# Optimization experiments

Measured on AMD Instinct MI355X. Metric: run time of the kernel, lower is better.

Reference implementation:

```python
import jax, jax.numpy as jnp
import numpy as np

D = 4096       # embed_dim
H = 16         # num_heads
HD = D // H    # head_dim = 256
MLP_H = int(D * 2.0)  # 8192
L_V = 2048
L_T = 1024
GAMMA = 0.6
NOISE_STD = 0.07
TEMP = 0.05
LN_EPS = 1e-5


def setup_inputs() -> dict:
    key = jax.random.key(0)
    ks = jax.random.split(key, 16)
    s = 0.02
    return {
        "vision_feature": jax.random.normal(ks[0], (L_V, D), jnp.float32),
        "text_embed": jax.random.normal(ks[1], (L_T, D), jnp.float32),
        "attention_mask": jnp.zeros((L_T,), jnp.float32),  # additive mask, 0 = attend
        "noise": jax.random.normal(ks[2], (L_V,), jnp.float32),
        "Wq": jax.random.normal(ks[3], (D, D), jnp.float32) * s,
        "bq": jnp.zeros((D,), jnp.float32),
        "Wk": jax.random.normal(ks[4], (D, D), jnp.float32) * s,
        "bk": jnp.zeros((D,), jnp.float32),
        "Wv": jax.random.normal(ks[5], (D, D), jnp.float32) * s,
        "bv": jnp.zeros((D,), jnp.float32),
        "Wo": jax.random.normal(ks[6], (D, D), jnp.float32) * s,
        "bo": jnp.zeros((D,), jnp.float32),
        "ln_w": jnp.ones((D,), jnp.float32),
        "ln_b": jnp.zeros((D,), jnp.float32),
        "W1": jax.random.normal(ks[7], (MLP_H, D), jnp.float32) * s,
        "b1": jnp.zeros((MLP_H,), jnp.float32),
        "W2": jax.random.normal(ks[8], (1, MLP_H), jnp.float32) * s,
        "b2": jnp.zeros((1,), jnp.float32),
    }


def reference(vision_feature, text_embed, attention_mask, noise,
              Wq, bq, Wk, bk, Wv, bv, Wo, bo, ln_w, ln_b, W1, b1, W2, b2):
    # --- cross attention (vision queries over text keys/values) ---
    q = (vision_feature @ Wq.T + bq).reshape(L_V, H, HD)
    k = (text_embed @ Wk.T + bk).reshape(L_T, H, HD)
    v = (text_embed @ Wv.T + bv).reshape(L_T, H, HD)
    logits = jnp.einsum('qhd,khd->hqk', q, k) / np.float32(np.sqrt(HD))
    logits = logits + attention_mask[None, None, :]  # additive attn_mask
    attn = jax.nn.softmax(logits, axis=-1)
    ctx = jnp.einsum('hqk,khd->qhd', attn, v).reshape(L_V, D)
    attn_out = ctx @ Wo.T + bo
    # --- residual + layernorm ---
    x = vision_feature + attn_out
    mu = jnp.mean(x, axis=-1, keepdims=True)
    var = jnp.mean(jnp.square(x - mu), axis=-1, keepdims=True)
    xn = (x - mu) / jnp.sqrt(var + LN_EPS) * ln_w + ln_b
    # --- tiny MLP scorer ---
    h = jax.nn.gelu(xn @ W1.T + b1, approximate=False)
    weight_scores = (h @ W2.T + b2)[:, 0] + noise * NOISE_STD
    # --- temperature softmax over all tokens, top-p (gamma) selection ---
    p = jax.nn.softmax(weight_scores / TEMP, axis=0)
    order = jnp.argsort(-p)           # descending sort indices
    cum = jnp.cumsum(p[order])
    keep = cum <= GAMMA               # threshold_index prefix mask
    gathered = vision_feature[order]  # [L_V, D]
    # fixed-shape stand-in for indices[:threshold_index] gather:
    # valid selected rows are the nonzero prefix
    return jnp.where(keep[:, None], gathered, jnp.zeros((), gathered.dtype))
```

## Files before the change

kernel.cpp:

```cpp
#include <hip/hip_runtime.h>
#include <math.h>


#define LV   2048
#define LT   1024
#define DIM  4096
#define NHD  16
#define HDD  256
#define MLPH 8192

typedef __attribute__((ext_vector_type(8))) short bfx8;
typedef __attribute__((ext_vector_type(4))) float fx4;
typedef unsigned short u16;

__device__ __forceinline__ float wave_sum(float v){
#pragma unroll
  for (int o = 32; o > 0; o >>= 1) v += __shfl_xor(v, o);
  return v;
}
__device__ __forceinline__ float wave_max(float v){
#pragma unroll
  for (int o = 32; o > 0; o >>= 1) v = fmaxf(v, __shfl_xor(v, o));
  return v;
}

__device__ __forceinline__ void splitpack(const float4 a, const float4 b,
                                          bfx8* hi, bfx8* lo){
  float f[8] = {a.x,a.y,a.z,a.w, b.x,b.y,b.z,b.w};
  union { bfx8 v; unsigned u[4]; } H, L;
#pragma unroll
  for (int p = 0; p < 4; ++p){
    unsigned u0 = __float_as_uint(f[2*p]);
    unsigned u1 = __float_as_uint(f[2*p+1]);
    H.u[p] = (u0 >> 16) | (u1 & 0xffff0000u);
    float h0 = __uint_as_float(u0 & 0xffff0000u);
    float h1 = __uint_as_float(u1 & 0xffff0000u);
    unsigned v0 = __float_as_uint(f[2*p]   - h0);
    unsigned v1 = __float_as_uint(f[2*p+1] - h1);
    L.u[p] = (v0 >> 16) | (v1 & 0xffff0000u);
  }
  *hi = H.v; *lo = L.v;
}

__device__ __forceinline__ void glds16(const void* g, void* l){
  __builtin_amdgcn_global_load_lds(
      (const __attribute__((address_space(1))) unsigned int*)g,
      (__attribute__((address_space(3))) unsigned int*)l, 16, 0, 0);
}

__global__ __launch_bounds__(256)
void repack_kernel(const float* __restrict__ src, u16* __restrict__ hi,
                   u16* __restrict__ lo, int Kc, int ktsh)
{
  const long long e = ((long long)blockIdx.x * 256 + threadIdx.x) * 8;
  const int T = (int)(e >> 9);
  const int L = (int)(e >> 3) & 63;
  const int rt = T >> ktsh, kt = T & ((1 << ktsh) - 1);
  const int r = (rt << 4) + (L & 15);
  const int k = (kt << 5) + ((L >> 4) << 3);
  const float* p = src + (long long)r * Kc + k;
  bfx8 h, l;
  splitpack(*(const float4*)p, *(const float4*)(p + 4), &h, &l);
  *(bfx8*)(hi + e) = h;
  *(bfx8*)(lo + e) = l;
}

template<int GELU, int TRANSC>
__global__ __launch_bounds__(256)
void mgemm(const u16* __restrict__ Ah, const u16* __restrict__ Al, int aKT, long long aZe,
           const u16* __restrict__ Bh, const u16* __restrict__ Bl, int bKT, long long bZe,
           float* __restrict__ C, int ldc, long long cZe,
           const float* __restrict__ bias,
           int nx, int KT, int kt0, int zkt, float alpha)
{
  __shared__ bfx8 lbuf[2][32][64];
  const int tid  = threadIdx.x;
  const int lane = tid & 63;
  const int wv   = tid >> 6;
  const int wr   = wv >> 1, wc = wv & 1;
  const int nwg  = gridDim.x;
  const int id   = blockIdx.x;
  int bm, bn;
  {
    const int my = nwg / nx;
    if (((nx & 3) == 0) && ((my & 1) == 0) && ((nwg & 7) == 0)){
      const int rm = my >> 1, rn = nx >> 2;
      const int x  = id & 7;
      const int j  = id >> 3;
      bm = ((x >> 2) * rm) + j / rn;
      bn = ((x & 3) * rn) + j % rn;
    } else if (((my & 7) == 0) && ((nwg & 7) == 0)){
      const int rm = my >> 3;
      const int x = id & 7, j = id >> 3;
      bm = x * rm + j / nx;
      bn = j % nx;
    } else { bm = id / nx; bn = id % nx; }
  }
  const int m0 = bm << 7;
  const int n0 = bn << 7;
  const int z    = blockIdx.z;
  const u16* Ahz = Ah + (long long)z * aZe;
  const u16* Alz = Al + (long long)z * aZe;
  const u16* Bhz = Bh + (long long)z * bZe;
  const u16* Blz = Bl + (long long)z * bZe;
  C += (long long)z * cZe;
  const int ktb  = kt0 + z * zkt;
  const int rtA0 = m0 >> 4, rtB0 = n0 >> 4;

  const fx4 zz = {0.f, 0.f, 0.f, 0.f};
  fx4 acc[4][4];
#pragma unroll
  for (int i = 0; i < 4; ++i)
#pragma unroll
    for (int j = 0; j < 4; ++j) acc[i][j] = zz;

  const u16* wbase = (wv == 0) ? Ahz : (wv == 1) ? Alz : (wv == 2) ? Bhz : Blz;
  const int  wrt0  = (wv < 2) ? rtA0 : rtB0;
  const int  wKT   = (wv < 2) ? aKT  : bKT;

#define STAGE(BUF, KTI)                                                        \
  {                                                                            \
    _Pragma("unroll")                                                          \
    for (int q = 0; q < 8; ++q){                                               \
      const u16* g = wbase + ((long long)(wrt0 + q) * wKT + (KTI)) * 512       \
                     + lane * 8;                                               \
      glds16((const void*)g, (void*)&lbuf[BUF][wv * 8 + q][0]);                \
    }                                                                          \
  }

  int cur = 0;
  STAGE(0, ktb);
  for (int t = 0; t < KT; ++t){
    __syncthreads();
    if (t + 1 < KT) STAGE(cur ^ 1, ktb + t + 1);
    bfx8 ah[4], al[4], bh[4], bl[4];
#pragma unroll
    for (int i = 0; i < 4; ++i){
      ah[i] = lbuf[cur][     wr*4 + i][lane];
      al[i] = lbuf[cur][ 8 + wr*4 + i][lane];
      bh[i] = lbuf[cur][16 + wc*4 + i][lane];
      bl[i] = lbuf[cur][24 + wc*4 + i][lane];
    }
#pragma unroll
    for (int i = 0; i < 4; ++i)
#pragma unroll
      for (int j = 0; j < 4; ++j){
        acc[i][j] = __builtin_amdgcn_mfma_f32_16x16x32_bf16(ah[i], bl[j], acc[i][j], 0, 0, 0);
        acc[i][j] = __builtin_amdgcn_mfma_f32_16x16x32_bf16(al[i], bh[j], acc[i][j], 0, 0, 0);
        acc[i][j] = __builtin_amdgcn_mfma_f32_16x16x32_bf16(ah[i], bh[j], acc[i][j], 0, 0, 0);
      }
    cur ^= 1;
  }
#undef STAGE

#pragma unroll
  for (int i = 0; i < 4; ++i){
    const int row0 = m0 + wr*64 + i*16 + ((lane >> 4) << 2);
#pragma unroll
    for (int j = 0; j < 4; ++j){
      const int col = n0 + wc*64 + j*16 + (lane & 15);
      const float bb = bias ? bias[col] : 0.0f;
      if (TRANSC){
        float4 o;
        o.x = alpha*acc[i][j][0] + bb;
        o.y = alpha*acc[i][j][1] + bb;
        o.z = alpha*acc[i][j][2] + bb;
        o.w = alpha*acc[i][j][3] + bb;
        *(float4*)(C + (size_t)col*ldc + row0) = o;
      } else {
#pragma unroll
        for (int r = 0; r < 4; ++r){
          float v = alpha*acc[i][j][r] + bb;
          if (GELU) v = 0.5f*v*(1.0f + erff(v*0.70710678f));
          C[(size_t)(row0 + r)*ldc + col] = v;
        }
      }
    }
  }
}

template<int GELU, int TRANSC>
__global__ __launch_bounds__(256)
void mgemm_fb(const float* __restrict__ A, long long aZ, int lda,
              const float* __restrict__ B, long long bZ, int ldb,
              float* __restrict__ C, long long cZ, int ldc,
              const float* __restrict__ bias, int Kd, float alpha)
{
  __shared__ bfx8 AhS[512], AlS[512], BhS[512], BlS[512];
  const int tid  = threadIdx.x;
  const int lane = tid & 63;
  const int wv   = tid >> 6;
  const int wr   = wv >> 1, wc = wv & 1;
  const int m0 = blockIdx.y * 128, n0 = blockIdx.x * 128;
  A += (long long)blockIdx.z * aZ;
  B += (long long)blockIdx.z * bZ;
  C += (long long)blockIdx.z * cZ;

  const fx4 zz = {0.f, 0.f, 0.f, 0.f};
  fx4 acc[4][4];
#pragma unroll
  for (int i = 0; i < 4; ++i)
#pragma unroll
    for (int j = 0; j < 4; ++j) acc[i][j] = zz;

  for (int k0 = 0; k0 < Kd; k0 += 32){
    __syncthreads();
#pragma unroll
    for (int pass = 0; pass < 2; ++pass){
      const int s = pass*256 + tid;
      const int m = ((s >> 6) << 4) + (s & 15);
      const int j = (s >> 4) & 3;
      const float* pA = A + (size_t)(m0 + m)*lda + k0 + j*8;
      splitpack(*(const float4*)pA, *(const float4*)(pA + 4), &AhS[s], &AlS[s]);
      const float* pB = B + (size_t)(n0 + m)*ldb + k0 + j*8;
      splitpack(*(const float4*)pB, *(const float4*)(pB + 4), &BhS[s], &BlS[s]);
    }
    __syncthreads();
    bfx8 ah[4], al[4], bh[4], bl[4];
#pragma unroll
    for (int i = 0; i < 4; ++i){
      ah[i] = AhS[(wr*4 + i)*64 + lane];
      al[i] = AlS[(wr*4 + i)*64 + lane];
      bh[i] = BhS[(wc*4 + i)*64 + lane];
      bl[i] = BlS[(wc*4 + i)*64 + lane];
    }
#pragma unroll
    for (int i = 0; i < 4; ++i)
#pragma unroll
      for (int j = 0; j < 4; ++j){
        acc[i][j] = __builtin_amdgcn_mfma_f32_16x16x32_bf16(ah[i], bl[j], acc[i][j], 0, 0, 0);
        acc[i][j] = __builtin_amdgcn_mfma_f32_16x16x32_bf16(al[i], bh[j], acc[i][j], 0, 0, 0);
        acc[i][j] = __builtin_amdgcn_mfma_f32_16x16x32_bf16(ah[i], bh[j], acc[i][j], 0, 0, 0);
      }
  }
#pragma unroll
  for (int i = 0; i < 4; ++i){
    const int row0 = m0 + wr*64 + i*16 + ((lane >> 4) << 2);
#pragma unroll
    for (int j = 0; j < 4; ++j){
      const int col = n0 + wc*64 + j*16 + (lane & 15);
      const float bb = bias ? bias[col] : 0.0f;
      if (TRANSC){
        float4 o;
        o.x = alpha*acc[i][j][0] + bb;
        o.y = alpha*acc[i][j][1] + bb;
        o.z = alpha*acc[i][j][2] + bb;
        o.w = alpha*acc[i][j][3] + bb;
        *(float4*)(C + (size_t)col*ldc + row0) = o;
      } else {
#pragma unroll
        for (int r = 0; r < 4; ++r){
          float v = alpha*acc[i][j][r] + bb;
          if (GELU) v = 0.5f*v*(1.0f + erff(v*0.70710678f));
          C[(size_t)(row0 + r)*ldc + col] = v;
        }
      }
    }
  }
}

__global__ __launch_bounds__(128)
void softmax_pack(const float* __restrict__ Lf, u16* __restrict__ ph,
                  u16* __restrict__ pl)
{
  __shared__ float rr[4];
  const int tid = threadIdx.x;
  const int h = blockIdx.x >> 11;
  const int m = blockIdx.x & 2047;
  const float* row = Lf + ((long long)h * 2048 + m) * 1024;
  const int k = tid * 8;
  float4 a = *(const float4*)(row + k);
  float4 b = *(const float4*)(row + k + 4);
  float v[8] = {a.x,a.y,a.z,a.w, b.x,b.y,b.z,b.w};
  float mx = v[0];
#pragma unroll
  for (int i = 1; i < 8; ++i) mx = fmaxf(mx, v[i]);
  mx = wave_max(mx);
  if ((tid & 63) == 0) rr[tid >> 6] = mx;
  __syncthreads();
  const float M = fmaxf(rr[0], rr[1]);
  float e[8], s = 0.0f;
#pragma unroll
  for (int i = 0; i < 8; ++i){ e[i] = expf(v[i] - M); s += e[i]; }
  s = wave_sum(s);
  if ((tid & 63) == 0) rr[2 + (tid >> 6)] = s;
  __syncthreads();
  const float S = rr[2] + rr[3];
  float4 p0 = make_float4(e[0]/S, e[1]/S, e[2]/S, e[3]/S);
  float4 p1 = make_float4(e[4]/S, e[5]/S, e[6]/S, e[7]/S);
  bfx8 hh, ll;
  splitpack(p0, p1, &hh, &ll);
  const int tile = (m >> 4) * 32 + (k >> 5);
  const int Lw = ((k >> 3) & 3) * 16 + (m & 15);
  const long long eoff = (long long)h * (2048ll*1024) + (long long)tile * 512 + Lw * 8;
  *(bfx8*)(ph + eoff) = hh;
  *(bfx8*)(pl + eoff) = ll;
}

__global__ __launch_bounds__(256)
void softmax_fb(float* __restrict__ X)
{
  __shared__ float r[8];
  const int tid = threadIdx.x;
  float* row = X + (size_t)blockIdx.x * 1024;
  float4 v = ((const float4*)row)[tid];
  float m = fmaxf(fmaxf(v.x,v.y), fmaxf(v.z,v.w));
  m = wave_max(m);
  if ((tid & 63) == 0) r[tid >> 6] = m;
  __syncthreads();
  m = fmaxf(fmaxf(r[0],r[1]), fmaxf(r[2],r[3]));
  float e0 = expf(v.x - m), e1 = expf(v.y - m), e2 = expf(v.z - m), e3 = expf(v.w - m);
  float s = (e0 + e1) + (e2 + e3);
  s = wave_sum(s);
  if ((tid & 63) == 0) r[4 + (tid >> 6)] = s;
  __syncthreads();
  s = (r[4] + r[5]) + (r[6] + r[7]);
  ((float4*)row)[tid] = make_float4(e0/s, e1/s, e2/s, e3/s);
}

template<int PACK>
__global__ __launch_bounds__(256)
void ln_kernel(const float* __restrict__ vis, const float* ao, float* xnf,
               u16* __restrict__ xh, u16* __restrict__ xl,
               const float* __restrict__ w, const float* __restrict__ b)
{
  __shared__ float r[8];
  __shared__ float stat[2];
  const int tid = threadIdx.x;
  const int m = blockIdx.x;
  const size_t base = (size_t)m * DIM + tid * 16;
  float x[16];
#pragma unroll
  for (int q = 0; q < 4; ++q){
    float4 a = *(const float4*)(vis + base + q*4);
    float4 c = *(const float4*)(ao  + base + q*4);
    x[q*4+0]=a.x+c.x; x[q*4+1]=a.y+c.y; x[q*4+2]=a.z+c.z; x[q*4+3]=a.w+c.w;
  }
  float s = 0.0f;
#pragma unroll
  for (int i = 0; i < 16; ++i) s += x[i];
  s = wave_sum(s);
  if ((tid & 63) == 0) r[tid >> 6] = s;
  __syncthreads();
  if (tid == 0) stat[0] = (r[0]+r[1]+r[2]+r[3]) * (1.0f/4096.0f);
  __syncthreads();
  const float mu = stat[0];
  float vs = 0.0f;
#pragma unroll
  for (int i = 0; i < 16; ++i){ float d = x[i]-mu; vs += d*d; }
  vs = wave_sum(vs);
  if ((tid & 63) == 0) r[4 + (tid >> 6)] = vs;
  __syncthreads();
  if (tid == 0) stat[1] = (r[4]+r[5]+r[6]+r[7]) * (1.0f/4096.0f);
  __syncthreads();
  const float inv = 1.0f / sqrtf(stat[1] + 1e-5f);
  const int col = tid * 16;
  float o[16];
#pragma unroll
  for (int q = 0; q < 4; ++q){
    float4 wv = *(const float4*)(w + col + q*4);
    float4 bv = *(const float4*)(b + col + q*4);
    o[q*4+0] = (x[q*4+0]-mu)*inv*wv.x + bv.x;
    o[q*4+1] = (x[q*4+1]-mu)*inv*wv.y + bv.y;
    o[q*4+2] = (x[q*4+2]-mu)*inv*wv.z + bv.z;
    o[q*4+3] = (x[q*4+3]-mu)*inv*wv.w + bv.w;
  }
  if (PACK){
#pragma unroll
    for (int q = 0; q < 2; ++q){
      const int k = col + q*8;
      float4 p0 = make_float4(o[q*8+0], o[q*8+1], o[q*8+2], o[q*8+3]);
      float4 p1 = make_float4(o[q*8+4], o[q*8+5], o[q*8+6], o[q*8+7]);
      bfx8 hh, ll;
      splitpack(p0, p1, &hh, &ll);
      const int tile = (m >> 4) * 128 + (k >> 5);
      const int Lw = ((k >> 3) & 3) * 16 + (m & 15);
      const long long e = (long long)tile * 512 + Lw * 8;
      *(bfx8*)(xh + e) = hh;
      *(bfx8*)(xl + e) = ll;
    }
  } else {
#pragma unroll
    for (int q = 0; q < 4; ++q)
      *(float4*)(xnf + base + q*4) = make_float4(o[q*4+0],o[q*4+1],o[q*4+2],o[q*4+3]);
  }
}

__global__ __launch_bounds__(256)
void score_kernel(const float* __restrict__ H1, const float* __restrict__ W2v,
                  const float* __restrict__ b2, const float* __restrict__ noise,
                  float* __restrict__ sc)
{
  __shared__ float r[4];
  const int tid = threadIdx.x;
  const float* h = H1 + (size_t)blockIdx.x * MLPH + tid * 32;
  const float* w = W2v + tid * 32;
  float s = 0.0f;
#pragma unroll
  for (int q = 0; q < 8; ++q){
    float4 a = *(const float4*)(h + q*4);
    float4 c = *(const float4*)(w + q*4);
    s += a.x*c.x + a.y*c.y + a.z*c.z + a.w*c.w;
  }
  s = wave_sum(s);
  if ((tid & 63) == 0) r[tid >> 6] = s;
  __syncthreads();
  if (tid == 0) sc[blockIdx.x] = (r[0]+r[1]+r[2]+r[3]) + b2[0] + noise[blockIdx.x]*0.07f;
}

__global__ __launch_bounds__(256)
void select_kernel(const float* __restrict__ scores,
                   int* __restrict__ ord, int* __restrict__ kcount)
{
  __shared__ float sv[LV];
  __shared__ int   si[LV];
  __shared__ float red[8];
  const int tid = threadIdx.x;
  for (int i = tid; i < LV; i += 256){ sv[i] = scores[i] / 0.05f; si[i] = i; }
  __syncthreads();
  float m = -3.4e38f;
  for (int i = tid; i < LV; i += 256) m = fmaxf(m, sv[i]);
  m = wave_max(m);
  if ((tid & 63) == 0) red[tid >> 6] = m;
  __syncthreads();
  const float ymax = fmaxf(fmaxf(red[0],red[1]), fmaxf(red[2],red[3]));
  float d = 0.0f;
  for (int i = tid; i < LV; i += 256) d += expf(sv[i] - ymax);
  d = wave_sum(d);
  if ((tid & 63) == 0) red[4 + (tid >> 6)] = d;
  __syncthreads();
  const float denom = (red[4]+red[5]) + (red[6]+red[7]);
  for (int size = 2; size <= LV; size <<= 1){
    for (int stride = size >> 1; stride > 0; stride >>= 1){
      __syncthreads();
      for (int t = tid; t < LV/2; t += 256){
        int i = 2*t - (t & (stride - 1));
        int j = i + stride;
        bool up = ((i & size) == 0);
        float a = sv[i], b = sv[j];
        if ((a < b) == up){
          sv[i] = b; sv[j] = a;
          int ti = si[i]; si[i] = si[j]; si[j] = ti;
        }
      }
    }
  }
  __syncthreads();
  for (int i = tid; i < LV; i += 256) sv[i] = expf(sv[i] - ymax) / denom;
  __syncthreads();
  if (tid == 0){
    float c = 0.0f; int kc = LV;
    for (int j = 0; j < LV; ++j){
      c += sv[j];
      if (!((double)c <= 0.6)){ kc = j; break; }
    }
    *kcount = kc;
  }
  __syncthreads();
  for (int i = tid; i < LV; i += 256) ord[i] = si[i];
}

__global__ __launch_bounds__(256)
void writer_kernel(const float* __restrict__ vis, const int* __restrict__ ord,
                   const int* __restrict__ kc, float* __restrict__ out)
{
  const int j = blockIdx.x;
  float4* dst = (float4*)(out + (size_t)j * DIM);
  if (j < kc[0]){
    const float4* src = (const float4*)(vis + (size_t)ord[j] * DIM);
    for (int i = threadIdx.x; i < DIM/4; i += 256) dst[i] = src[i];
  } else {
    const float4 z4 = make_float4(0.f,0.f,0.f,0.f);
    for (int i = threadIdx.x; i < DIM/4; i += 256) dst[i] = z4;
  }
}

extern "C" void kernel_launch(void* const* d_in, const int* in_sizes, int n_in,
                              void* d_out, int out_size, void* d_ws, size_t ws_size,
                              hipStream_t stream)
{
  (void)in_sizes; (void)n_in; (void)out_size;
  const float* vis  = (const float*)d_in[0];
  const float* txt  = (const float*)d_in[1];
  const float* mask = (const float*)d_in[2];
  const float* noise= (const float*)d_in[3];
  const float* Wq = (const float*)d_in[4];  const float* bq = (const float*)d_in[5];
  const float* Wk = (const float*)d_in[6];  const float* bk = (const float*)d_in[7];
  const float* Wv = (const float*)d_in[8];  const float* bv = (const float*)d_in[9];
  const float* Wo = (const float*)d_in[10]; const float* bo = (const float*)d_in[11];
  const float* lw = (const float*)d_in[12]; const float* lb = (const float*)d_in[13];
  const float* W1 = (const float*)d_in[14]; const float* b1 = (const float*)d_in[15];
  const float* W2 = (const float*)d_in[16]; const float* b2 = (const float*)d_in[17];
  float* out = (float*)d_out;
  const dim3 blk(256);
  const size_t MiB = 1u << 20;

  int Hc = 0;
  for (int h = 16; h >= 1; h >>= 1){
    size_t need = (192 + 16 * (size_t)h) * MiB;
    if (need <= ws_size){ Hc = h; break; }
  }

  if (Hc > 0){
    char* B0 = (char*)d_ws;
    u16* WSh  = (u16*)(B0 + 0);          u16* WSl  = (u16*)(B0 + 32*MiB);
    float* TMPf = (float*)(B0 + 64*MiB);
    u16* QCh  = (u16*)(B0 + 96*MiB);     u16* QCl  = (u16*)(B0 + 112*MiB);
    u16* VCh  = (u16*)(B0 + 128*MiB);    u16* VCl  = (u16*)(B0 + 144*MiB);
    u16* TCh  = (u16*)(B0 + 160*MiB);    u16* TCl  = (u16*)(B0 + 168*MiB);
    float* KF  = (float*)(B0 + 176*MiB);
    float* VTF = (float*)(B0 + 192*MiB);
    u16* VTCh = (u16*)(B0 + 176*MiB);    u16* VTCl = (u16*)(B0 + 184*MiB);
    float* Lf  = (float*)(B0 + 192*MiB);
    u16* PCh  = (u16*)(B0 + (192 + (size_t)Hc*8)*MiB);
    u16* PCl  = (u16*)(B0 + (192 + (size_t)Hc*12)*MiB);
    float* H1f = (float*)(B0 + 128*MiB);
    u16* XNh  = (u16*)(B0 + 96*MiB);     u16* XNl  = (u16*)(B0 + 112*MiB);
    float* SCf = (float*)(B0 + 192*MiB);
    int* ORD = (int*)(SCf + LV);
    int* KCp = ORD + LV;

    repack_kernel<<<dim3(4096), blk, 0, stream>>>(vis, VCh, VCl, 4096, 7);
    repack_kernel<<<dim3(2048), blk, 0, stream>>>(txt, TCh, TCl, 4096, 7);
    repack_kernel<<<dim3(8192), blk, 0, stream>>>(Wq, WSh, WSl, 4096, 7);
    mgemm<0,0><<<dim3(512,1,1), blk, 0, stream>>>(VCh, VCl, 128, 0, WSh, WSl, 128, 0,
        TMPf, 4096, 0, bq, 32, 128, 0, 0, 1.0f);
    repack_kernel<<<dim3(8192), blk, 0, stream>>>(Wk, WSh, WSl, 4096, 7);
    mgemm<0,0><<<dim3(256,1,1), blk, 0, stream>>>(TCh, TCl, 128, 0, WSh, WSl, 128, 0,
        KF, 4096, 0, bk, 32, 128, 0, 0, 1.0f);
    repack_kernel<<<dim3(8192), blk, 0, stream>>>(Wv, WSh, WSl, 4096, 7);
    mgemm<0,1><<<dim3(256,1,1), blk, 0, stream>>>(TCh, TCl, 128, 0, WSh, WSl, 128, 0,
        VTF, 1024, 0, bv, 32, 128, 0, 0, 1.0f);
    repack_kernel<<<dim3(4096), blk, 0, stream>>>(TMPf, QCh, QCl, 4096, 7);
    repack_kernel<<<dim3(2048), blk, 0, stream>>>(KF, TCh, TCl, 4096, 7);
    repack_kernel<<<dim3(2048), blk, 0, stream>>>(VTF, VTCh, VTCl, 1024, 5);
    const int NG = NHD / Hc;
    for (int g = 0; g < NG; ++g){
      mgemm<0,0><<<dim3(128,1,Hc), blk, 0, stream>>>(QCh, QCl, 128, 0, TCh, TCl, 128, 0,
          Lf, 1024, 2097152ll, mask, 8, 8, g*Hc*8, 8, 0.0625f);
      softmax_pack<<<dim3(Hc*2048), dim3(128), 0, stream>>>(Lf, PCh, PCl);
      mgemm<0,0><<<dim3(32,1,Hc), blk, 0, stream>>>(PCh, PCl, 32, 2097152ll,
          VTCh + (long long)g*Hc*262144, VTCl + (long long)g*Hc*262144, 32, 262144ll,
          TMPf + (long long)g*Hc*256, 4096, 256, nullptr, 2, 32, 0, 0, 1.0f);
    }
    repack_kernel<<<dim3(4096), blk, 0, stream>>>(TMPf, VCh, VCl, 4096, 7);
    repack_kernel<<<dim3(8192), blk, 0, stream>>>(Wo, WSh, WSl, 4096, 7);
    mgemm<0,0><<<dim3(512,1,1), blk, 0, stream>>>(VCh, VCl, 128, 0, WSh, WSl, 128, 0,
        TMPf, 4096, 0, bo, 32, 128, 0, 0, 1.0f);
    ln_kernel<1><<<dim3(LV), blk, 0, stream>>>(vis, TMPf, nullptr, XNh, XNl, lw, lb);
    repack_kernel<<<dim3(8192), blk, 0, stream>>>(W1, WSh, WSl, 4096, 7);
    mgemm<1,0><<<dim3(512,1,1), blk, 0, stream>>>(XNh, XNl, 128, 0, WSh, WSl, 128, 0,
        H1f, 8192, 0, b1, 32, 128, 0, 0, 1.0f);
    repack_kernel<<<dim3(8192), blk, 0, stream>>>(W1 + 16777216ll, WSh, WSl, 4096, 7);
    mgemm<1,0><<<dim3(512,1,1), blk, 0, stream>>>(XNh, XNl, 128, 0, WSh, WSl, 128, 0,
        H1f + 4096, 8192, 0, b1 + 4096, 32, 128, 0, 0, 1.0f);
    score_kernel<<<dim3(LV), blk, 0, stream>>>(H1f, W2, b2, noise, SCf);
    select_kernel<<<dim3(1), blk, 0, stream>>>(SCf, ORD, KCp);
    writer_kernel<<<dim3(LV), blk, 0, stream>>>(vis, ORD, KCp, out);
    return;
  }

  float* ws = (float*)d_ws;
  const long long OQ  = 0;
  const long long OK_ = (long long)LV * DIM;
  const long long OV  = OK_ + (long long)LT * DIM;
  const long long OC  = OV  + (long long)LT * DIM;
  const long long OL  = OC  + (long long)LV * DIM;
  const long long LSTRIDE = (long long)LV * LT;
  int Hf = 16;
  while (Hf > 1){
    size_t need = (size_t)(OL + (long long)Hf * LSTRIDE + 8192) * 4;
    if (need <= ws_size) break;
    Hf >>= 1;
  }
  float* Qw  = ws + OQ;
  float* Kw  = ws + OK_;
  float* Vt  = ws + OV;
  float* Cw  = ws + OC;
  float* Lw  = ws + OL;
  float* H1w = ws + OK_;
  float* SCw = ws + OL + (long long)Hf * LSTRIDE;
  int*   ORDw = (int*)(SCw + LV);
  int*   KCw  = ORDw + LV;

  mgemm_fb<0,0><<<dim3(DIM/128, LV/128, 1), blk, 0, stream>>>(vis,0,DIM, Wq,0,DIM, Qw,0,DIM, bq, DIM, 1.0f);
  mgemm_fb<0,0><<<dim3(DIM/128, LT/128, 1), blk, 0, stream>>>(txt,0,DIM, Wk,0,DIM, Kw,0,DIM, bk, DIM, 1.0f);
  mgemm_fb<0,1><<<dim3(DIM/128, LT/128, 1), blk, 0, stream>>>(txt,0,DIM, Wv,0,DIM, Vt,0,LT, bv, DIM, 1.0f);
  for (int g = 0; g < NHD/Hf; ++g){
    const long long ho = (long long)g * Hf * HDD;
    mgemm_fb<0,0><<<dim3(LT/128, LV/128, Hf), blk, 0, stream>>>(
        Qw+ho, HDD, DIM,  Kw+ho, HDD, DIM,  Lw, LSTRIDE, LT,  mask, HDD, 0.0625f);
    softmax_fb<<<dim3(Hf*LV), blk, 0, stream>>>(Lw);
    mgemm_fb<0,0><<<dim3(HDD/128, LV/128, Hf), blk, 0, stream>>>(
        Lw, LSTRIDE, LT,  Vt + (ho*(long long)LT), (long long)HDD*LT, LT,
        Cw+ho, HDD, DIM,  nullptr, LT, 1.0f);
  }
  mgemm_fb<0,0><<<dim3(DIM/128, LV/128, 1), blk, 0, stream>>>(Cw,0,DIM, Wo,0,DIM, Qw,0,DIM, bo, DIM, 1.0f);
  ln_kernel<0><<<dim3(LV), blk, 0, stream>>>(vis, Qw, Qw, nullptr, nullptr, lw, lb);
  mgemm_fb<1,0><<<dim3(MLPH/128, LV/128, 1), blk, 0, stream>>>(Qw,0,DIM, W1,0,DIM, H1w,0,MLPH, b1, DIM, 1.0f);
  score_kernel<<<dim3(LV), blk, 0, stream>>>(H1w, W2, b2, noise, SCw);
  select_kernel<<<dim3(1), blk, 0, stream>>>(SCw, ORDw, KCw);
  writer_kernel<<<dim3(LV), blk, 0, stream>>>(vis, ORDw, KCw, out);
}
```

Measured before the change: 1.459 ms.

## Single-buffer GEMM LDS staging and widen select kernel to 1024 threads

The mgemm main loop drops its double-buffered LDS prefetch. Each iteration now loads one k-tile into a single buffer, syncs, computes, and syncs again. This halves LDS use per block, which may allow more resident blocks, but global loads no longer overlap with MFMA work. Separately, the single-block select kernel runs with 1024 threads so each bitonic compare-exchange step needs one pass per thread instead of four, with reductions widened to 16 waves.

Result: slower. 1.643 ms (+12.6%).

```diff
diff --git a/kernel.cpp b/kernel.cpp
--- a/kernel.cpp
+++ b/kernel.cpp
@@ -73,7 +73,7 @@
            const float* __restrict__ bias,
            int nx, int KT, int kt0, int zkt, float alpha)
 {
-  __shared__ bfx8 lbuf[2][32][64];
+  __shared__ bfx8 lbuf[32][64];
   const int tid  = threadIdx.x;
   const int lane = tid & 63;
   const int wv   = tid >> 6;
@@ -118,28 +118,21 @@
   const int  wrt0  = (wv < 2) ? rtA0 : rtB0;
   const int  wKT   = (wv < 2) ? aKT  : bKT;
 
-#define STAGE(BUF, KTI)                                                        \
-  {                                                                            \
-    _Pragma("unroll")                                                          \
-    for (int q = 0; q < 8; ++q){                                               \
-      const u16* g = wbase + ((long long)(wrt0 + q) * wKT + (KTI)) * 512       \
-                     + lane * 8;                                               \
-      glds16((const void*)g, (void*)&lbuf[BUF][wv * 8 + q][0]);                \
-    }                                                                          \
-  }
-
-  int cur = 0;
-  STAGE(0, ktb);
   for (int t = 0; t < KT; ++t){
+#pragma unroll
+    for (int q = 0; q < 8; ++q){
+      const u16* g = wbase + ((long long)(wrt0 + q) * wKT + (ktb + t)) * 512
+                     + lane * 8;
+      glds16((const void*)g, (void*)&lbuf[wv * 8 + q][0]);
+    }
     __syncthreads();
-    if (t + 1 < KT) STAGE(cur ^ 1, ktb + t + 1);
     bfx8 ah[4], al[4], bh[4], bl[4];
 #pragma unroll
     for (int i = 0; i < 4; ++i){
-      ah[i] = lbuf[cur][     wr*4 + i][lane];
-      al[i] = lbuf[cur][ 8 + wr*4 + i][lane];
-      bh[i] = lbuf[cur][16 + wc*4 + i][lane];
-      bl[i] = lbuf[cur][24 + wc*4 + i][lane];
+      ah[i] = lbuf[     wr*4 + i][lane];
+      al[i] = lbuf[ 8 + wr*4 + i][lane];
+      bh[i] = lbuf[16 + wc*4 + i][lane];
+      bl[i] = lbuf[24 + wc*4 + i][lane];
     }
 #pragma unroll
     for (int i = 0; i < 4; ++i)
@@ -149,9 +142,8 @@
         acc[i][j] = __builtin_amdgcn_mfma_f32_16x16x32_bf16(al[i], bh[j], acc[i][j], 0, 0, 0);
         acc[i][j] = __builtin_amdgcn_mfma_f32_16x16x32_bf16(ah[i], bh[j], acc[i][j], 0, 0, 0);
       }
-    cur ^= 1;
-  }
-#undef STAGE
+    __syncthreads();
+  }
 
 #pragma unroll
   for (int i = 0; i < 4; ++i){
@@ -408,45 +400,56 @@
   if (tid == 0) sc[blockIdx.x] = (r[0]+r[1]+r[2]+r[3]) + b2[0] + noise[blockIdx.x]*0.07f;
 }
 
-__global__ __launch_bounds__(256)
+__global__ __launch_bounds__(1024)
 void select_kernel(const float* __restrict__ scores,
                    int* __restrict__ ord, int* __restrict__ kcount)
 {
   __shared__ float sv[LV];
   __shared__ int   si[LV];
-  __shared__ float red[8];
+  __shared__ float red[32];
+  __shared__ float stat[2];
   const int tid = threadIdx.x;
-  for (int i = tid; i < LV; i += 256){ sv[i] = scores[i] / 0.05f; si[i] = i; }
+  for (int i = tid; i < LV; i += 1024){ sv[i] = scores[i] / 0.05f; si[i] = i; }
   __syncthreads();
   float m = -3.4e38f;
-  for (int i = tid; i < LV; i += 256) m = fmaxf(m, sv[i]);
+  for (int i = tid; i < LV; i += 1024) m = fmaxf(m, sv[i]);
   m = wave_max(m);
   if ((tid & 63) == 0) red[tid >> 6] = m;
   __syncthreads();
-  const float ymax = fmaxf(fmaxf(red[0],red[1]), fmaxf(red[2],red[3]));
+  if (tid == 0){
+    float M = red[0];
+    for (int w = 1; w < 16; ++w) M = fmaxf(M, red[w]);
+    stat[0] = M;
+  }
+  __syncthreads();
+  const float ymax = stat[0];
   float d = 0.0f;
-  for (int i = tid; i < LV; i += 256) d += expf(sv[i] - ymax);
+  for (int i = tid; i < LV; i += 1024) d += expf(sv[i] - ymax);
   d = wave_sum(d);
-  if ((tid & 63) == 0) red[4 + (tid >> 6)] = d;
-  __syncthreads();
-  const float denom = (red[4]+red[5]) + (red[6]+red[7]);
+  if ((tid & 63) == 0) red[16 + (tid >> 6)] = d;
+  __syncthreads();
+  if (tid == 0){
+    float D = 0.0f;
+    for (int w = 0; w < 16; ++w) D += red[16 + w];
+    stat[1] = D;
+  }
+  __syncthreads();
+  const float denom = stat[1];
   for (int size = 2; size <= LV; size <<= 1){
     for (int stride = size >> 1; stride > 0; stride >>= 1){
       __syncthreads();
-      for (int t = tid; t < LV/2; t += 256){
-        int i = 2*t - (t & (stride - 1));
-        int j = i + stride;
-        bool up = ((i & size) == 0);
-        float a = sv[i], b = sv[j];
-        if ((a < b) == up){
-          sv[i] = b; sv[j] = a;
-          int ti = si[i]; si[i] = si[j]; si[j] = ti;
-        }
+      const int i = 2*tid - (tid & (stride - 1));
+      const int j = i + stride;
+      const bool up = ((i & size) == 0);
+      float a = sv[i], b = sv[j];
+      if ((a < b) == up){
+        sv[i] = b; sv[j] = a;
+        int ti = si[i]; si[i] = si[j]; si[j] = ti;
       }
     }
   }
   __syncthreads();
-  for (int i = tid; i < LV; i += 256) sv[i] = expf(sv[i] - ymax) / denom;
+  for (int i = tid; i < LV; i += 1024) sv[i] = expf(sv[i] - ymax) / denom;
   __syncthreads();
   if (tid == 0){
     float c = 0.0f; int kc = LV;
@@ -457,7 +460,7 @@
     *kcount = kc;
   }
   __syncthreads();
-  for (int i = tid; i < LV; i += 256) ord[i] = si[i];
+  for (int i = tid; i < LV; i += 1024) ord[i] = si[i];
 }
 
 __global__ __launch_bounds__(256)
@@ -555,7 +558,7 @@
     mgemm<1,0><<<dim3(512,1,1), blk, 0, stream>>>(XNh, XNl, 128, 0, WSh, WSl, 128, 0,
         H1f + 4096, 8192, 0, b1 + 4096, 32, 128, 0, 0, 1.0f);
     score_kernel<<<dim3(LV), blk, 0, stream>>>(H1f, W2, b2, noise, SCf);
-    select_kernel<<<dim3(1), blk, 0, stream>>>(SCf, ORD, KCp);
+    select_kernel<<<dim3(1), dim3(1024), 0, stream>>>(SCf, ORD, KCp);
     writer_kernel<<<dim3(LV), blk, 0, stream>>>(vis, ORD, KCp, out);
     return;
   }
@@ -599,6 +602,6 @@
   ln_kernel<0><<<dim3(LV), blk, 0, stream>>>(vis, Qw, Qw, nullptr, nullptr, lw, lb);
   mgemm_fb<1,0><<<dim3(MLPH/128, LV/128, 1), blk, 0, stream>>>(Qw,0,DIM, W1,0,DIM, H1w,0,MLPH, b1, DIM, 1.0f);
   score_kernel<<<dim3(LV), blk, 0, stream>>>(H1w, W2, b2, noise, SCw);
-  select_kernel<<<dim3(1), blk, 0, stream>>>(SCw, ORDw, KCw);
+  select_kernel<<<dim3(1), dim3(1024), 0, stream>>>(SCw, ORDw, KCw);
   writer_kernel<<<dim3(LV), blk, 0, stream>>>(vis, ORDw, KCw, out);
 }
```
